# Performance work log

Hardware: AMD Instinct MI355X
Metric: run time of the kernel (lower is better)

The kernel has to match this reference:

```python
import jax, jax.numpy as jnp
import numpy as np

EMBED_DIM = 1024
B, S = 4, 2048

def setup_inputs() -> dict:
    key = jax.random.key(0)
    ks = jax.random.split(key, 9)
    D = EMBED_DIM
    scale = 1.0 / np.sqrt(D)
    scale2 = 1.0 / np.sqrt(2 * D)
    return {
        "classical_state": jax.random.normal(ks[0], (B, S, D), jnp.float32),
        "quantum_state": jax.random.normal(ks[1], (B, S, D), jnp.float32),
        "Wc": jax.random.uniform(ks[2], (D, D), jnp.float32, -scale, scale),
        "bc": jax.random.uniform(ks[3], (D,), jnp.float32, -scale, scale),
        "Wq": jax.random.uniform(ks[4], (D, D), jnp.float32, -scale, scale),
        "bq": jax.random.uniform(ks[5], (D,), jnp.float32, -scale, scale),
        "Wg": jax.random.uniform(ks[6], (D, 2 * D), jnp.float32, -scale2, scale2),
        "bg": jax.random.uniform(ks[7], (D,), jnp.float32, -scale2, scale2),
        "temperature": jnp.array(1.0, jnp.float32),
    }

def reference(classical_state, quantum_state, Wc, bc, Wq, bq, Wg, bg, temperature):
    D = classical_state.shape[-1]
    c_proj = jnp.einsum('bsd,ed->bse', classical_state, Wc) + bc  # [B,S,D]
    q_proj = jnp.einsum('bsd,ed->bse', quantum_state, Wq) + bq    # [B,S,D]
    combined = jnp.concatenate([c_proj, q_proj], axis=-1)         # [B,S,2D]
    interface_state = jax.nn.sigmoid(jnp.einsum('bsf,ef->bse', combined, Wg) + bg)
    similarity = jnp.einsum('bsd,btd->bst', c_proj, q_proj) / jnp.sqrt(jnp.asarray(D, c_proj.dtype))
    attention_weights = jax.nn.softmax(similarity / temperature, axis=-1)  # [B,S,S]
    transfer_state = jnp.einsum('bst,btd->bsd', attention_weights, quantum_state)
    return classical_state + interface_state * transfer_state
```

## Files before the change

kernel.cpp:

```cpp
#include <hip/hip_runtime.h>


typedef unsigned short u16;
typedef unsigned char u8;
typedef __bf16 bf16x8 __attribute__((ext_vector_type(8)));
typedef float f32x4 __attribute__((ext_vector_type(4)));
typedef int i32x4 __attribute__((ext_vector_type(4)));
typedef int i32x8 __attribute__((ext_vector_type(8)));
typedef short short8 __attribute__((ext_vector_type(8)));

__device__ __forceinline__ u16 f2bf(float f) {
    unsigned int x;
    __builtin_memcpy(&x, &f, 4);
    unsigned int r = x + 0x7FFFu + ((x >> 16) & 1u);
    return (u16)(r >> 16);
}
__device__ __forceinline__ float bf2f(u16 u) {
    unsigned int x = ((unsigned int)u) << 16;
    float f;
    __builtin_memcpy(&f, &x, 4);
    return f;
}
__device__ __forceinline__ u8 f2fp8(float f) {
    int p = __builtin_amdgcn_cvt_pk_fp8_f32(f, f, 0, false);
    return (u8)(p & 0xFF);
}

__device__ __forceinline__ void xcd_tile(int& tx, int& ty) {
    const int gx = gridDim.x;
    const int nwg = gx * gridDim.y;
    const int l = blockIdx.x + gx * blockIdx.y;
    const int per = nwg >> 3;
    const int swz = (l & 7) * per + (l >> 3);
    tx = swz % gx;
    ty = swz / gx;
}

#define GLOBAL_TO_LDS16(gp, lp)                                                           \
    __builtin_amdgcn_global_load_lds((const __attribute__((address_space(1))) void*)(gp), \
                                     (__attribute__((address_space(3))) void*)(lp), 16, 0, 0)

__global__ __launch_bounds__(256, 2) void gemm_proj(
    const u16* __restrict__ Ac, const u16* __restrict__ Aq, int lda,
    const u16* __restrict__ Bp, long sBz, int ldb,
    u8* __restrict__ C8, long sCz, int ldc, int K,
    const float* __restrict__ bc, const float* __restrict__ bq) {
    __shared__ __align__(16) u16 As[2][128 * 64];
    __shared__ __align__(16) u16 Bs[2][128 * 64];

    const int tid  = threadIdx.x;
    const int lane = tid & 63;
    const int wave = tid >> 6;
    const int z    = blockIdx.z;

    const u16* a = z ? Aq : Ac;
    const u16* b = Bp + (long)z * sBz;
    const float* bias = z ? bq : bc;

    int tx, ty;
    xcd_tile(tx, ty);
    const int tileM = ty * 128;
    const int tileN = tx * 128;

    const int wm  = wave >> 1;
    const int wn  = wave & 1;
    const int r16 = lane & 15;
    const int kg  = lane >> 4;

    const int srow = lane >> 3;
    const int sgc  = ((lane & 7) ^ (lane >> 3)) * 8;
    const int swb  = r16 & 7;

    auto stage = [&](int buf, int t) {
        const int k0 = t * 64;
#pragma unroll
        for (int p = 0; p < 4; p++) {
            const int rbase = p * 32 + wave * 8;
            GLOBAL_TO_LDS16(a + (long)(tileM + rbase + srow) * lda + k0 + sgc, &As[buf][rbase * 64]);
            GLOBAL_TO_LDS16(b + (long)(tileN + rbase + srow) * ldb + k0 + sgc, &Bs[buf][rbase * 64]);
        }
    };

    f32x4 acc[4][4] = {};

    const int nt = K / 64;
    stage(0, 0);
    stage(1, 1);

    for (int t = 0; t < nt; t++) {
        const int cur = t & 1;
        if (t + 1 < nt) asm volatile("s_waitcnt vmcnt(8)" ::: "memory");
        else            asm volatile("s_waitcnt vmcnt(0)" ::: "memory");
        __builtin_amdgcn_s_barrier();
        asm volatile("" ::: "memory");

        bf16x8 af[2][4], bfr[2][4];
#pragma unroll
        for (int h = 0; h < 2; h++) {
#pragma unroll
            for (int i = 0; i < 4; i++) {
                const int Ra = wm * 64 + i * 16 + r16;
                af[h][i]  = *(const bf16x8*)&As[cur][Ra * 64 + (((h * 4 + kg) ^ swb)) * 8];
                const int Rb = wn * 64 + i * 16 + r16;
                bfr[h][i] = *(const bf16x8*)&Bs[cur][Rb * 64 + (((h * 4 + kg) ^ swb)) * 8];
            }
        }
#pragma unroll
        for (int h = 0; h < 2; h++)
#pragma unroll
            for (int i = 0; i < 4; i++)
#pragma unroll
                for (int j = 0; j < 4; j++)
                    acc[i][j] = __builtin_amdgcn_mfma_f32_16x16x32_bf16(
                        af[h][i], bfr[h][j], acc[i][j], 0, 0, 0);

        asm volatile("" ::: "memory");
        __builtin_amdgcn_s_barrier();
        if (t + 2 < nt) stage(cur, t + 2);
    }

#pragma unroll
    for (int i = 0; i < 4; i++)
#pragma unroll
        for (int j = 0; j < 4; j++) {
            int col = tileN + wn * 64 + j * 16 + r16;
            float bv = bias[col];
#pragma unroll
            for (int v = 0; v < 4; v++) {
                int row = tileM + wm * 64 + i * 16 + kg * 4 + v;
                C8[(long)z * sCz + (long)row * ldc + col] = f2fp8(acc[i][j][v] + bv);
            }
        }
}

template <int MODE>
__device__ __forceinline__ void gemm8_body(
    int tileM, int tileN, int z, int tid,
    const u8* __restrict__ A0, const u8* __restrict__ A1, long sAz, int lda, int kSplit,
    const u8* __restrict__ Bp, long sBz, int ldb,
    void* __restrict__ Cp, long cOff, long sCz, int ldc, int K,
    const float* __restrict__ bias, const float* __restrict__ temp,
    const float* __restrict__ cls, const u16* __restrict__ g16,
    float* __restrict__ lsum, long lSz,
    u8* As, u8* Bs) {
    const int lane = tid & 63;
    const int wave = tid >> 6;

    const u8* a = A0 + (long)z * sAz;
    const u8* b = Bp + (long)z * sBz;

    const int wm  = wave >> 1;
    const int wn  = wave & 1;
    const int r16 = lane & 15;
    const int kg  = lane >> 4;

    const int srow = lane >> 3;
    const int sgc  = ((lane & 7) ^ (lane >> 3)) * 16;

    f32x4 acc[4][4] = {};

    for (int k0 = 0; k0 < K; k0 += 128) {
        const u8* Ap = a;
        int kA = k0;
        if (MODE == 1 && k0 >= kSplit) { Ap = A1; kA = k0 - kSplit; }

#pragma unroll
        for (int p = 0; p < 4; p++) {
            const int rbase = p * 32 + wave * 8;
            GLOBAL_TO_LDS16(Ap + (long)(tileM + rbase + srow) * lda + kA + sgc, &As[rbase * 128]);
            GLOBAL_TO_LDS16(b + (long)(tileN + rbase + srow) * ldb + k0 + sgc, &Bs[rbase * 128]);
        }
        __syncthreads();

        i32x8 af[4];
#pragma unroll
        for (int i = 0; i < 4; i++) {
            const int Ra = wm * 64 + i * 16 + r16;
            const u8* base = &As[Ra * 128];
            *(i32x4*)&af[i]       = *(const i32x4*)&base[(((2 * kg)     ^ (Ra & 7))) * 16];
            *((i32x4*)&af[i] + 1) = *(const i32x4*)&base[(((2 * kg + 1) ^ (Ra & 7))) * 16];
        }
#pragma unroll
        for (int j = 0; j < 4; j++) {
            const int Rb = wn * 64 + j * 16 + r16;
            const u8* base = &Bs[Rb * 128];
            i32x8 bfr;
            *(i32x4*)&bfr       = *(const i32x4*)&base[(((2 * kg)     ^ (Rb & 7))) * 16];
            *((i32x4*)&bfr + 1) = *(const i32x4*)&base[(((2 * kg + 1) ^ (Rb & 7))) * 16];
#pragma unroll
            for (int i = 0; i < 4; i++)
                acc[i][j] = __builtin_amdgcn_mfma_scale_f32_16x16x128_f8f6f4(
                    af[i], bfr, acc[i][j], 0, 0, 0, 127, 0, 127);
        }
        __syncthreads();
    }

    u16*   C16 = (u16*)Cp;
    u8*    C8  = (u8*)Cp;
    float* C32 = (float*)Cp;

    if constexpr (MODE == 2) {
        const float scale = 1.0f / (32.0f * temp[0]);
        u8* Cs = As;
#pragma unroll
        for (int i = 0; i < 4; i++) {
            float rs[4] = {0.f, 0.f, 0.f, 0.f};
#pragma unroll
            for (int j = 0; j < 4; j++) {
                const int lcol = wn * 64 + j * 16 + r16;
#pragma unroll
                for (int v = 0; v < 4; v++) {
                    const int lrow = wm * 64 + i * 16 + kg * 4 + v;
                    float e = __expf(acc[i][j][v] * scale);
                    Cs[lrow * 128 + (lcol ^ ((lrow & 12) << 2))] = f2fp8(e);
                    rs[v] += e;
                }
            }
#pragma unroll
            for (int v = 0; v < 4; v++) {
                float s = rs[v];
#pragma unroll
                for (int off = 1; off < 16; off <<= 1) s += __shfl_xor(s, off, 64);
                if (r16 == 0) {
                    int row = tileM + wm * 64 + i * 16 + kg * 4 + v;
                    atomicAdd(&lsum[(long)z * lSz + row], s);
                }
            }
        }
        __syncthreads();
        const int r  = tid >> 1;
        const int ch = (tid & 1) * 64;
        const int rk = (r >> 2) & 3;
        i32x4 w[4];
#pragma unroll
        for (int m = 0; m < 4; m++)
            w[m] = *(const i32x4*)&Cs[r * 128 + ch + ((m ^ rk) << 4)];
        long base = cOff + (long)z * sCz + (long)(tileM + r) * ldc + tileN + ch;
#pragma unroll
        for (int m = 0; m < 4; m++)
            *(i32x4*)&C8[base + m * 16] = w[m];
    } else {
#pragma unroll
        for (int i = 0; i < 4; i++) {
#pragma unroll
            for (int j = 0; j < 4; j++) {
                int col = tileN + wn * 64 + j * 16 + r16;
                float bv = (MODE == 1) ? bias[col] : 0.0f;
#pragma unroll
                for (int v = 0; v < 4; v++) {
                    int row = tileM + wm * 64 + i * 16 + kg * 4 + v;
                    long idx = cOff + (long)z * sCz + (long)row * ldc + col;
                    float val = acc[i][j][v];
                    if (MODE == 1) {
                        C16[idx] = f2bf(1.0f / (1.0f + __expf(-(val + bv))));
                    } else {
                        float inv = 1.0f / lsum[(long)z * lSz + row];
                        C32[idx] = cls[idx] + bf2f(g16[idx]) * (val * inv);
                    }
                }
            }
        }
    }
}

template <int MODE>
__global__ __launch_bounds__(256, 2) void gemm8(
    const u8* __restrict__ A0, const u8* __restrict__ A1, long sAz, int lda, int kSplit,
    const u8* __restrict__ Bp, long sBz, int ldb,
    void* __restrict__ Cp, long cOff, long sCz, int ldc, int K,
    const float* __restrict__ bias, const float* __restrict__ temp,
    const float* __restrict__ cls, const u16* __restrict__ g16,
    float* __restrict__ lsum, long lSz) {
    __shared__ __align__(16) u8 As[128 * 128];
    __shared__ __align__(16) u8 Bs[128 * 128];
    int tx, ty;
    xcd_tile(tx, ty);
    gemm8_body<MODE>(ty * 128, tx * 128, blockIdx.z, threadIdx.x,
                     A0, A1, sAz, lda, kSplit, Bp, sBz, ldb,
                     Cp, cOff, sCz, ldc, K, bias, temp, cls, g16, lsum, lSz, As, Bs);
}

__global__ __launch_bounds__(256, 2) void gateSim(
    const u8* __restrict__ cp8, const u8* __restrict__ qp8,
    const u8* __restrict__ Wg8, u16* __restrict__ g, const float* __restrict__ bg,
    u8* __restrict__ P8, long sP, const float* __restrict__ temp,
    float* __restrict__ lsum, long lSz,
    long sBD, int D, int S, int nwgSim) {
    __shared__ __align__(16) u8 As[128 * 128];
    __shared__ __align__(16) u8 Bs[128 * 128];
    const int bid = blockIdx.x;
    if (bid < 512) {
        const int swz = (bid & 7) * 64 + (bid >> 3);
        const int tx = swz & 7, ty = swz >> 3;
        gemm8_body<1>(ty * 128, tx * 128, 0, threadIdx.x,
                      cp8, qp8, 0, D, D, Wg8, 0, 2 * D,
                      g, 0, 0, D, 2 * D,
                      bg, nullptr, nullptr, nullptr, nullptr, 0, As, Bs);
    } else {
        const int sb  = bid - 512;
        const int z   = sb / nwgSim;
        const int lid = sb - z * nwgSim;
        const int per = nwgSim >> 3;
        const int swz = (lid & 7) * per + (lid >> 3);
        const int tx = swz & 15, ty = swz >> 4;
        gemm8_body<2>(ty * 128, tx * 128, z, threadIdx.x,
                      cp8, nullptr, sBD, D, 1 << 30, qp8, sBD, D,
                      P8, 0, sP, S, D,
                      nullptr, temp, nullptr, nullptr, lsum, lSz, As, Bs);
    }
}

__global__ __launch_bounds__(256) void prepT(
    const f32x4* __restrict__ cls, const f32x4* __restrict__ qnt,
    const f32x4* __restrict__ Wc, const f32x4* __restrict__ Wq, const f32x4* __restrict__ Wg,
    ushort4* __restrict__ clsB, ushort4* __restrict__ qntB,
    ushort4* __restrict__ WcB, ushort4* __restrict__ WqB, unsigned int* __restrict__ Wg8,
    f32x4* __restrict__ l, long nM, long nW, long nG, long nL,
    const float* __restrict__ Qf, u8* __restrict__ QT, int S, int D) {
    __shared__ __align__(16) u8 tile[64][80];
    const int bid = blockIdx.x;
    if (bid < 2048) {
        long i = (long)bid * 256 + threadIdx.x;
        const long stride = 2048L * 256;
        const long total = 2 * nM + 2 * nW + nG + nL;
        for (; i < total; i += stride) {
            if (i < 2 * nM) {
                long j = (i < nM) ? i : i - nM;
                f32x4 v = (i < nM) ? cls[j] : qnt[j];
                ushort4 o;
                o.x = f2bf(v.x); o.y = f2bf(v.y); o.z = f2bf(v.z); o.w = f2bf(v.w);
                if (i < nM) clsB[j] = o; else qntB[j] = o;
            } else if (i < 2 * nM + 2 * nW) {
                long j = i - 2 * nM;
                long k = (j < nW) ? j : j - nW;
                f32x4 v = (j < nW) ? Wc[k] : Wq[k];
                ushort4 o;
                o.x = f2bf(v.x); o.y = f2bf(v.y); o.z = f2bf(v.z); o.w = f2bf(v.w);
                if (j < nW) WcB[k] = o; else WqB[k] = o;
            } else if (i < 2 * nM + 2 * nW + nG) {
                long j = i - 2 * nM - 2 * nW;
                f32x4 v = Wg[j];
                int w = __builtin_amdgcn_cvt_pk_fp8_f32(v.x, v.y, 0, false);
                w = __builtin_amdgcn_cvt_pk_fp8_f32(v.z, v.w, w, true);
                Wg8[j] = (unsigned int)w;
            } else {
                l[i - 2 * nM - 2 * nW - nG] = (f32x4){0.f, 0.f, 0.f, 0.f};
            }
        }
    } else {
        const int tb = bid - 2048;
        const int bx = tb & 31;
        const int by = (tb >> 5) & 15;
        const int bz = tb >> 9;
        const float* q = Qf + (long)bz * S * D;
        u8* qt = QT + (long)bz * S * D;
        const int t0 = bx * 64, d0 = by * 64;
        {
            const int r  = threadIdx.x >> 2;
            const int dc = (threadIdx.x & 3) * 16;
            const float* src = q + (long)(t0 + r) * D + d0 + dc;
            unsigned int pk[4];
#pragma unroll
            for (int m = 0; m < 4; m++) {
                f32x4 v = *(const f32x4*)(src + 4 * m);
                int w = __builtin_amdgcn_cvt_pk_fp8_f32(v.x, v.y, 0, false);
                w = __builtin_amdgcn_cvt_pk_fp8_f32(v.z, v.w, w, true);
                pk[m] = (unsigned int)w;
            }
            *(i32x4*)&tile[r][dc] = *(i32x4*)pk;
        }
        __syncthreads();
        {
            const int dl = threadIdx.x >> 2;
            const int tc = (threadIdx.x & 3) * 16;
            unsigned int w[4];
#pragma unroll
            for (int m = 0; m < 4; m++) {
                unsigned int x = 0;
#pragma unroll
                for (int k = 0; k < 4; k++)
                    x |= (unsigned int)tile[tc + m * 4 + k][dl] << (8 * k);
                w[m] = x;
            }
            *(i32x4*)&qt[(long)(d0 + dl) * S + t0 + tc] = *(i32x4*)w;
        }
    }
}

extern "C" void kernel_launch(void* const* d_in, const int* in_sizes, int n_in,
                              void* d_out, int out_size, void* d_ws, size_t ws_size,
                              hipStream_t stream) {
    (void)in_sizes; (void)n_in; (void)out_size;

    const float* classical = (const float*)d_in[0];
    const float* quantum   = (const float*)d_in[1];
    const float* Wc        = (const float*)d_in[2];
    const float* bc        = (const float*)d_in[3];
    const float* Wq        = (const float*)d_in[4];
    const float* bq        = (const float*)d_in[5];
    const float* Wg        = (const float*)d_in[6];
    const float* bg        = (const float*)d_in[7];
    const float* temp      = (const float*)d_in[8];
    float* out = (float*)d_out;

    const int B = 4, S = 2048, D = 1024;
    const long MD = (long)B * S * D;

    float* l    = (float*)d_ws;
    u16* Wc_b   = (u16*)(l + (long)B * S);
    u16* Wq_b   = Wc_b + (long)D * D;
    u8*  Wg8    = (u8*)(Wq_b + (long)D * D);
    u16* cls_b  = (u16*)(Wg8 + (long)D * 2 * D);
    u16* qnt_b  = cls_b + MD;
    u8*  cp8    = (u8*)(qnt_b + MD);
    u8*  qp8    = cp8 + MD;
    u8*  qT8    = qp8 + MD;
    u8*  P8     = qT8 + MD;
    u16* g      = cls_b;

    const size_t fixed_bytes = (size_t)B * S * 4 + 2 * (size_t)D * D * 2 +
        (size_t)D * 2 * D + 2 * (size_t)MD * 2 + 3 * (size_t)MD;
    int CH = 128;
    for (int c = 2048; c >= 128; c >>= 1) {
        if (ws_size >= fixed_bytes + (size_t)B * c * S) { CH = c; break; }
    }
    const int chDiv  = CH / 128;
    const int nwgSim = (S / 128) * chDiv;

    dim3 blk(256);

    prepT<<<4096, blk, 0, stream>>>(
        (const f32x4*)classical, (const f32x4*)quantum,
        (const f32x4*)Wc, (const f32x4*)Wq, (const f32x4*)Wg,
        (ushort4*)cls_b, (ushort4*)qnt_b,
        (ushort4*)Wc_b, (ushort4*)Wq_b, (unsigned int*)Wg8,
        (f32x4*)l, MD / 4, (long)D * D / 4, (long)D * 2 * D / 4, (long)B * S / 4,
        quantum, qT8, S, D);

    gemm_proj<<<dim3(D / 128, (B * S) / 128, 2), blk, 0, stream>>>(
        cls_b, qnt_b, D, Wc_b, (long)D * D, D, cp8, MD, D, D, bc, bq);

    gateSim<<<512 + B * nwgSim, blk, 0, stream>>>(
        cp8, qp8, Wg8, g, bg,
        P8, (long)CH * S, temp, l, S,
        (long)S * D, D, S, nwgSim);

    gemm8<4><<<dim3(D / 128, chDiv, B), blk, 0, stream>>>(
        P8, nullptr, (long)CH * S, S, 1 << 30, qT8, (long)D * S, S,
        out, 0, (long)S * D, D, S,
        nullptr, nullptr, classical, g, l, S);

    for (int m0 = CH; m0 < S; m0 += CH) {
        gemm8<2><<<dim3(S / 128, chDiv, B), blk, 0, stream>>>(
            cp8 + (long)m0 * D, nullptr, (long)S * D, D, 1 << 30,
            qp8, (long)S * D, D, P8, 0, (long)CH * S, S, D,
            nullptr, temp, nullptr, nullptr, l + m0, S);
        gemm8<4><<<dim3(D / 128, chDiv, B), blk, 0, stream>>>(
            P8, nullptr, (long)CH * S, S, 1 << 30, qT8, (long)D * S, S,
            out, (long)m0 * D, (long)S * D, D, S,
            nullptr, nullptr, classical, g, l + m0, S);
    }
}
```

Before: 247.7 us.

## Fuse gate, similarity and PV GEMMs into persistent kernel with atomic counters

Adds a persistent 512-block kernel that computes the similarity tiles and gate GEMM, signals completion through global atomic counters, then runs the P·V output GEMM. The output stage spin-waits on the gate counter only before its epilogue, so its main loop can overlap with gate work. This removes the separate launches and the tail bubble between them when the workspace holds the full S×S matrix. It also drops __restrict__ on GEMM arguments and rewrites the fp8 transpose to pack 4-byte columns in shared memory. The cost is a dependency on spin-wait progress: this assumes all 512 blocks are co-resident, otherwise it can deadlock.

```diff
diff --git a/kernel.cpp b/kernel.cpp
--- a/kernel.cpp
+++ b/kernel.cpp
@@ -7,7 +7,6 @@
 typedef float f32x4 __attribute__((ext_vector_type(4)));
 typedef int i32x4 __attribute__((ext_vector_type(4)));
 typedef int i32x8 __attribute__((ext_vector_type(8)));
-typedef short short8 __attribute__((ext_vector_type(8)));
 
 __device__ __forceinline__ u16 f2bf(float f) {
     unsigned int x;
@@ -133,16 +132,16 @@
         }
 }
 
-template <int MODE>
+template <int MODE, bool WAITG>
 __device__ __forceinline__ void gemm8_body(
     int tileM, int tileN, int z, int tid,
-    const u8* __restrict__ A0, const u8* __restrict__ A1, long sAz, int lda, int kSplit,
-    const u8* __restrict__ Bp, long sBz, int ldb,
-    void* __restrict__ Cp, long cOff, long sCz, int ldc, int K,
-    const float* __restrict__ bias, const float* __restrict__ temp,
-    const float* __restrict__ cls, const u16* __restrict__ g16,
-    float* __restrict__ lsum, long lSz,
-    u8* As, u8* Bs) {
+    const u8* A0, const u8* A1, long sAz, int lda, int kSplit,
+    const u8* Bp, long sBz, int ldb,
+    void* Cp, long cOff, long sCz, int ldc, int K,
+    const float* bias, const float* temp,
+    const float* cls, const u16* g16,
+    float* lsum, long lSz,
+    u8* As, u8* Bs, unsigned int* gDone) {
     const int lane = tid & 63;
     const int wave = tid >> 6;
 
@@ -191,6 +190,15 @@
             for (int i = 0; i < 4; i++)
                 acc[i][j] = __builtin_amdgcn_mfma_scale_f32_16x16x128_f8f6f4(
                     af[i], bfr, acc[i][j], 0, 0, 0, 127, 0, 127);
+        }
+        __syncthreads();
+    }
+
+    if constexpr (WAITG) {
+        if (tid == 0) {
+            while (__hip_atomic_load(gDone, __ATOMIC_RELAXED, __HIP_MEMORY_SCOPE_AGENT) < 512u)
+                __builtin_amdgcn_s_sleep(2);
+            __threadfence();
         }
         __syncthreads();
     }
@@ -265,26 +273,27 @@
 
 template <int MODE>
 __global__ __launch_bounds__(256, 2) void gemm8(
-    const u8* __restrict__ A0, const u8* __restrict__ A1, long sAz, int lda, int kSplit,
-    const u8* __restrict__ Bp, long sBz, int ldb,
-    void* __restrict__ Cp, long cOff, long sCz, int ldc, int K,
-    const float* __restrict__ bias, const float* __restrict__ temp,
-    const float* __restrict__ cls, const u16* __restrict__ g16,
-    float* __restrict__ lsum, long lSz) {
+    const u8* A0, const u8* A1, long sAz, int lda, int kSplit,
+    const u8* Bp, long sBz, int ldb,
+    void* Cp, long cOff, long sCz, int ldc, int K,
+    const float* bias, const float* temp,
+    const float* cls, const u16* g16,
+    float* lsum, long lSz) {
     __shared__ __align__(16) u8 As[128 * 128];
     __shared__ __align__(16) u8 Bs[128 * 128];
     int tx, ty;
     xcd_tile(tx, ty);
-    gemm8_body<MODE>(ty * 128, tx * 128, blockIdx.z, threadIdx.x,
-                     A0, A1, sAz, lda, kSplit, Bp, sBz, ldb,
-                     Cp, cOff, sCz, ldc, K, bias, temp, cls, g16, lsum, lSz, As, Bs);
+    gemm8_body<MODE, false>(ty * 128, tx * 128, blockIdx.z, threadIdx.x,
+                            A0, A1, sAz, lda, kSplit, Bp, sBz, ldb,
+                            Cp, cOff, sCz, ldc, K, bias, temp, cls, g16, lsum, lSz,
+                            As, Bs, nullptr);
 }
 
 __global__ __launch_bounds__(256, 2) void gateSim(
-    const u8* __restrict__ cp8, const u8* __restrict__ qp8,
-    const u8* __restrict__ Wg8, u16* __restrict__ g, const float* __restrict__ bg,
-    u8* __restrict__ P8, long sP, const float* __restrict__ temp,
-    float* __restrict__ lsum, long lSz,
+    const u8* cp8, const u8* qp8,
+    const u8* Wg8, u16* g, const float* bg,
+    u8* P8, long sP, const float* temp,
+    float* lsum, long lSz,
     long sBD, int D, int S, int nwgSim) {
     __shared__ __align__(16) u8 As[128 * 128];
     __shared__ __align__(16) u8 Bs[128 * 128];
@@ -292,10 +301,10 @@
     if (bid < 512) {
         const int swz = (bid & 7) * 64 + (bid >> 3);
         const int tx = swz & 7, ty = swz >> 3;
-        gemm8_body<1>(ty * 128, tx * 128, 0, threadIdx.x,
-                      cp8, qp8, 0, D, D, Wg8, 0, 2 * D,
-                      g, 0, 0, D, 2 * D,
-                      bg, nullptr, nullptr, nullptr, nullptr, 0, As, Bs);
+        gemm8_body<1, false>(ty * 128, tx * 128, 0, threadIdx.x,
+                             cp8, qp8, 0, D, D, Wg8, 0, 2 * D,
+                             g, 0, 0, D, 2 * D,
+                             bg, nullptr, nullptr, nullptr, nullptr, 0, As, Bs, nullptr);
     } else {
         const int sb  = bid - 512;
         const int z   = sb / nwgSim;
@@ -303,10 +312,66 @@
         const int per = nwgSim >> 3;
         const int swz = (lid & 7) * per + (lid >> 3);
         const int tx = swz & 15, ty = swz >> 4;
-        gemm8_body<2>(ty * 128, tx * 128, z, threadIdx.x,
-                      cp8, nullptr, sBD, D, 1 << 30, qp8, sBD, D,
-                      P8, 0, sP, S, D,
-                      nullptr, temp, nullptr, nullptr, lsum, lSz, As, Bs);
+        gemm8_body<2, false>(ty * 128, tx * 128, z, threadIdx.x,
+                             cp8, nullptr, sBD, D, 1 << 30, qp8, sBD, D,
+                             P8, 0, sP, S, D,
+                             nullptr, temp, nullptr, nullptr, lsum, lSz, As, Bs, nullptr);
+    }
+}
+
+__global__ __launch_bounds__(256, 2) void megaGSP(
+    const u8* cp8, const u8* qp8, const u8* Wg8, void* g, const float* bg,
+    void* P8, const float* temp, float* lsum,
+    const u8* qT8, const float* cls, void* out,
+    unsigned int* syncc, int D, int S) {
+    __shared__ __align__(16) u8 As[128 * 128];
+    __shared__ __align__(16) u8 Bs[128 * 128];
+    const int b   = blockIdx.x;
+    const int tid = threadIdx.x;
+    const long sBD = (long)S * D;
+
+#pragma unroll 1
+    for (int it = 0; it < 3; it++) {
+        const int k = b + it * 512;
+        if (k < 1024) {
+            const int z = k >> 8, lid = k & 255;
+            const int swz = (lid & 7) * 32 + (lid >> 3);
+            gemm8_body<2, false>((swz >> 4) * 128, (swz & 15) * 128, z, tid,
+                                 cp8, nullptr, sBD, D, 1 << 30, qp8, sBD, D,
+                                 P8, 0, (long)S * S, S, D,
+                                 nullptr, temp, nullptr, nullptr, lsum, S, As, Bs, nullptr);
+            __syncthreads();
+            if (tid == 0)
+                __hip_atomic_fetch_add(&syncc[0], 1u, __ATOMIC_RELEASE, __HIP_MEMORY_SCOPE_AGENT);
+        } else {
+            const int lid = k - 1024;
+            const int swz = (lid & 7) * 64 + (lid >> 3);
+            gemm8_body<1, false>((swz >> 3) * 128, (swz & 7) * 128, 0, tid,
+                                 cp8, qp8, 0, D, D, Wg8, 0, 2 * D,
+                                 g, 0, 0, D, 2 * D,
+                                 bg, nullptr, nullptr, nullptr, nullptr, 0, As, Bs, nullptr);
+            __syncthreads();
+            if (tid == 0)
+                __hip_atomic_fetch_add(&syncc[1], 1u, __ATOMIC_RELEASE, __HIP_MEMORY_SCOPE_AGENT);
+        }
+    }
+
+    if (tid == 0) {
+        while (__hip_atomic_load(&syncc[0], __ATOMIC_RELAXED, __HIP_MEMORY_SCOPE_AGENT) < 1024u)
+            __builtin_amdgcn_s_sleep(2);
+        __threadfence();
+    }
+    __syncthreads();
+
+    {
+        const int z = b >> 7, lid = b & 127;
+        const int swz = (lid & 7) * 16 + (lid >> 3);
+        gemm8_body<4, true>((swz >> 3) * 128, (swz & 7) * 128, z, tid,
+                            (const u8*)P8, nullptr, (long)S * S, S, 1 << 30,
+                            qT8, (long)D * S, S,
+                            out, 0, sBD, D, S,
+                            nullptr, nullptr, cls, (const u16*)g, lsum, S,
+                            As, Bs, &syncc[1]);
     }
 }
 
@@ -316,9 +381,11 @@
     ushort4* __restrict__ clsB, ushort4* __restrict__ qntB,
     ushort4* __restrict__ WcB, ushort4* __restrict__ WqB, unsigned int* __restrict__ Wg8,
     f32x4* __restrict__ l, long nM, long nW, long nG, long nL,
-    const float* __restrict__ Qf, u8* __restrict__ QT, int S, int D) {
-    __shared__ __align__(16) u8 tile[64][80];
+    const float* __restrict__ Qf, u8* __restrict__ QT, int S, int D,
+    unsigned int* __restrict__ syncc) {
+    __shared__ unsigned int tile2[64][17];
     const int bid = blockIdx.x;
+    if (bid == 0 && threadIdx.x < 4) syncc[threadIdx.x] = 0;
     if (bid < 2048) {
         long i = (long)bid * 256 + threadIdx.x;
         const long stride = 2048L * 256;
@@ -356,33 +423,28 @@
         u8* qt = QT + (long)bz * S * D;
         const int t0 = bx * 64, d0 = by * 64;
         {
-            const int r  = threadIdx.x >> 2;
-            const int dc = (threadIdx.x & 3) * 16;
-            const float* src = q + (long)(t0 + r) * D + d0 + dc;
-            unsigned int pk[4];
-#pragma unroll
-            for (int m = 0; m < 4; m++) {
-                f32x4 v = *(const f32x4*)(src + 4 * m);
-                int w = __builtin_amdgcn_cvt_pk_fp8_f32(v.x, v.y, 0, false);
-                w = __builtin_amdgcn_cvt_pk_fp8_f32(v.z, v.w, w, true);
-                pk[m] = (unsigned int)w;
-            }
-            *(i32x4*)&tile[r][dc] = *(i32x4*)pk;
+            const int dg = threadIdx.x & 15;
+            const int tg = threadIdx.x >> 4;
+            unsigned int col[4] = {0u, 0u, 0u, 0u};
+#pragma unroll
+            for (int r = 0; r < 4; r++) {
+                f32x4 v = *(const f32x4*)(q + (long)(t0 + tg * 4 + r) * D + d0 + dg * 4);
+                col[0] |= (unsigned int)f2fp8(v.x) << (8 * r);
+                col[1] |= (unsigned int)f2fp8(v.y) << (8 * r);
+                col[2] |= (unsigned int)f2fp8(v.z) << (8 * r);
+                col[3] |= (unsigned int)f2fp8(v.w) << (8 * r);
+            }
+#pragma unroll
+            for (int j = 0; j < 4; j++) tile2[dg * 4 + j][tg] = col[j];
         }
         __syncthreads();
         {
-            const int dl = threadIdx.x >> 2;
-            const int tc = (threadIdx.x & 3) * 16;
-            unsigned int w[4];
-#pragma unroll
-            for (int m = 0; m < 4; m++) {
-                unsigned int x = 0;
-#pragma unroll
-                for (int k = 0; k < 4; k++)
-                    x |= (unsigned int)tile[tc + m * 4 + k][dl] << (8 * k);
-                w[m] = x;
-            }
-            *(i32x4*)&qt[(long)(d0 + dl) * S + t0 + tc] = *(i32x4*)w;
+            const int dr = threadIdx.x >> 2;
+            const int mq = threadIdx.x & 3;
+            i32x4 w;
+#pragma unroll
+            for (int k = 0; k < 4; k++) w[k] = (int)tile2[dr][mq * 4 + k];
+            *(i32x4*)&qt[(long)(d0 + dr) * S + t0 + mq * 16] = w;
         }
     }
 }
@@ -422,10 +484,9 @@
         (size_t)D * 2 * D + 2 * (size_t)MD * 2 + 3 * (size_t)MD;
     int CH = 128;
     for (int c = 2048; c >= 128; c >>= 1) {
-        if (ws_size >= fixed_bytes + (size_t)B * c * S) { CH = c; break; }
-    }
-    const int chDiv  = CH / 128;
-    const int nwgSim = (S / 128) * chDiv;
+        if (ws_size >= fixed_bytes + (size_t)B * c * S + 64) { CH = c; break; }
+    }
+    unsigned int* syncc = (unsigned int*)(P8 + (size_t)B * CH * S);
 
     dim3 blk(256);
 
@@ -435,29 +496,35 @@
         (ushort4*)cls_b, (ushort4*)qnt_b,
         (ushort4*)Wc_b, (ushort4*)Wq_b, (unsigned int*)Wg8,
         (f32x4*)l, MD / 4, (long)D * D / 4, (long)D * 2 * D / 4, (long)B * S / 4,
-        quantum, qT8, S, D);
+        quantum, qT8, S, D, syncc);
 
     gemm_proj<<<dim3(D / 128, (B * S) / 128, 2), blk, 0, stream>>>(
         cls_b, qnt_b, D, Wc_b, (long)D * D, D, cp8, MD, D, D, bc, bq);
 
-    gateSim<<<512 + B * nwgSim, blk, 0, stream>>>(
-        cp8, qp8, Wg8, g, bg,
-        P8, (long)CH * S, temp, l, S,
-        (long)S * D, D, S, nwgSim);
-
-    gemm8<4><<<dim3(D / 128, chDiv, B), blk, 0, stream>>>(
-        P8, nullptr, (long)CH * S, S, 1 << 30, qT8, (long)D * S, S,
-        out, 0, (long)S * D, D, S,
-        nullptr, nullptr, classical, g, l, S);
-
-    for (int m0 = CH; m0 < S; m0 += CH) {
-        gemm8<2><<<dim3(S / 128, chDiv, B), blk, 0, stream>>>(
-            cp8 + (long)m0 * D, nullptr, (long)S * D, D, 1 << 30,
-            qp8, (long)S * D, D, P8, 0, (long)CH * S, S, D,
-            nullptr, temp, nullptr, nullptr, l + m0, S);
+    if (CH == S) {
+        megaGSP<<<512, blk, 0, stream>>>(
+            cp8, qp8, Wg8, g, bg, P8, temp, l, qT8, classical, out,
+            syncc, D, S);
+    } else {
+        const int chDiv  = CH / 128;
+        const int nwgSim = (S / 128) * chDiv;
+        gateSim<<<512 + B * nwgSim, blk, 0, stream>>>(
+            cp8, qp8, Wg8, g, bg,
+            P8, (long)CH * S, temp, l, S,
+            (long)S * D, D, S, nwgSim);
         gemm8<4><<<dim3(D / 128, chDiv, B), blk, 0, stream>>>(
             P8, nullptr, (long)CH * S, S, 1 << 30, qT8, (long)D * S, S,
-            out, (long)m0 * D, (long)S * D, D, S,
-            nullptr, nullptr, classical, g, l + m0, S);
-    }
-}
+            out, 0, (long)S * D, D, S,
+            nullptr, nullptr, classical, g, l, S);
+        for (int m0 = CH; m0 < S; m0 += CH) {
+            gemm8<2><<<dim3(S / 128, chDiv, B), blk, 0, stream>>>(
+                cp8 + (long)m0 * D, nullptr, (long)S * D, D, 1 << 30,
+                qp8, (long)S * D, D, P8, 0, (long)CH * S, S, D,
+                nullptr, temp, nullptr, nullptr, l + m0, S);
+            gemm8<4><<<dim3(D / 128, chDiv, B), blk, 0, stream>>>(
+                P8, nullptr, (long)CH * S, S, 1 << 30, qT8, (long)D * S, S,
+                out, (long)m0 * D, (long)S * D, D, S,
+                nullptr, nullptr, classical, g, l + m0, S);
+        }
+    }
+}
```

New measurement: 365.6 us. 47.6% more time.

## Move quantum-state FP8 transpose from prep kernel into gate/similarity launch

Applied to the files above, without the earlier changes.

The transpose-and-quantize of the quantum state to FP8 (qT8) moves out of the prep kernel and runs as extra trailing blocks of the gateSim launch, with a new LDS layout that packs four tokens per word and reads 16-byte rows. The prep kernel shrinks to the elementwise conversions, so the transpose work can overlap with the gate and similarity GEMM tail instead of lengthening the first kernel. The __restrict__ qualifiers are also dropped from the GEMM signatures, which may change how the compiler schedules loads. The extra blocks could contend with the GEMM tiles for CUs, and the transpose still has to finish before the later PV GEMM, which reads qT8.

```diff
diff --git a/kernel.cpp b/kernel.cpp
--- a/kernel.cpp
+++ b/kernel.cpp
@@ -7,7 +7,6 @@
 typedef float f32x4 __attribute__((ext_vector_type(4)));
 typedef int i32x4 __attribute__((ext_vector_type(4)));
 typedef int i32x8 __attribute__((ext_vector_type(8)));
-typedef short short8 __attribute__((ext_vector_type(8)));
 
 __device__ __forceinline__ u16 f2bf(float f) {
     unsigned int x;
@@ -136,12 +135,12 @@
 template <int MODE>
 __device__ __forceinline__ void gemm8_body(
     int tileM, int tileN, int z, int tid,
-    const u8* __restrict__ A0, const u8* __restrict__ A1, long sAz, int lda, int kSplit,
-    const u8* __restrict__ Bp, long sBz, int ldb,
-    void* __restrict__ Cp, long cOff, long sCz, int ldc, int K,
-    const float* __restrict__ bias, const float* __restrict__ temp,
-    const float* __restrict__ cls, const u16* __restrict__ g16,
-    float* __restrict__ lsum, long lSz,
+    const u8* A0, const u8* A1, long sAz, int lda, int kSplit,
+    const u8* Bp, long sBz, int ldb,
+    void* Cp, long cOff, long sCz, int ldc, int K,
+    const float* bias, const float* temp,
+    const float* cls, const u16* g16,
+    float* lsum, long lSz,
     u8* As, u8* Bs) {
     const int lane = tid & 63;
     const int wave = tid >> 6;
@@ -265,12 +264,12 @@
 
 template <int MODE>
 __global__ __launch_bounds__(256, 2) void gemm8(
-    const u8* __restrict__ A0, const u8* __restrict__ A1, long sAz, int lda, int kSplit,
-    const u8* __restrict__ Bp, long sBz, int ldb,
-    void* __restrict__ Cp, long cOff, long sCz, int ldc, int K,
-    const float* __restrict__ bias, const float* __restrict__ temp,
-    const float* __restrict__ cls, const u16* __restrict__ g16,
-    float* __restrict__ lsum, long lSz) {
+    const u8* A0, const u8* A1, long sAz, int lda, int kSplit,
+    const u8* Bp, long sBz, int ldb,
+    void* Cp, long cOff, long sCz, int ldc, int K,
+    const float* bias, const float* temp,
+    const float* cls, const u16* g16,
+    float* lsum, long lSz) {
     __shared__ __align__(16) u8 As[128 * 128];
     __shared__ __align__(16) u8 Bs[128 * 128];
     int tx, ty;
@@ -281,32 +280,68 @@
 }
 
 __global__ __launch_bounds__(256, 2) void gateSim(
-    const u8* __restrict__ cp8, const u8* __restrict__ qp8,
-    const u8* __restrict__ Wg8, u16* __restrict__ g, const float* __restrict__ bg,
-    u8* __restrict__ P8, long sP, const float* __restrict__ temp,
-    float* __restrict__ lsum, long lSz,
-    long sBD, int D, int S, int nwgSim) {
+    const u8* cp8, const u8* qp8,
+    const u8* Wg8, u16* g, const float* bg,
+    u8* P8, long sP, const float* temp,
+    float* lsum, long lSz,
+    long sBD, int D, int S, int nwgSim,
+    const float* Qf, u8* qT8) {
     __shared__ __align__(16) u8 As[128 * 128];
     __shared__ __align__(16) u8 Bs[128 * 128];
     const int bid = blockIdx.x;
+    const int tid = threadIdx.x;
+    const int gemmEnd = 512 + 4 * nwgSim;
     if (bid < 512) {
         const int swz = (bid & 7) * 64 + (bid >> 3);
         const int tx = swz & 7, ty = swz >> 3;
-        gemm8_body<1>(ty * 128, tx * 128, 0, threadIdx.x,
+        gemm8_body<1>(ty * 128, tx * 128, 0, tid,
                       cp8, qp8, 0, D, D, Wg8, 0, 2 * D,
                       g, 0, 0, D, 2 * D,
                       bg, nullptr, nullptr, nullptr, nullptr, 0, As, Bs);
-    } else {
+    } else if (bid < gemmEnd) {
         const int sb  = bid - 512;
         const int z   = sb / nwgSim;
         const int lid = sb - z * nwgSim;
         const int per = nwgSim >> 3;
         const int swz = (lid & 7) * per + (lid >> 3);
         const int tx = swz & 15, ty = swz >> 4;
-        gemm8_body<2>(ty * 128, tx * 128, z, threadIdx.x,
+        gemm8_body<2>(ty * 128, tx * 128, z, tid,
                       cp8, nullptr, sBD, D, 1 << 30, qp8, sBD, D,
                       P8, 0, sP, S, D,
                       nullptr, temp, nullptr, nullptr, lsum, lSz, As, Bs);
+    } else {
+        const int tb = bid - gemmEnd;
+        const int bx = tb & 31;
+        const int by = (tb >> 5) & 15;
+        const int bz = tb >> 9;
+        unsigned int (*tile2)[17] = (unsigned int(*)[17])As;
+        const float* q = Qf + (long)bz * S * D;
+        u8* qt = qT8 + (long)bz * S * D;
+        const int t0 = bx * 64, d0 = by * 64;
+        {
+            const int dg = tid & 15;
+            const int tg = tid >> 4;
+            unsigned int col[4] = {0u, 0u, 0u, 0u};
+#pragma unroll
+            for (int r = 0; r < 4; r++) {
+                f32x4 v = *(const f32x4*)(q + (long)(t0 + tg * 4 + r) * D + d0 + dg * 4);
+                col[0] |= (unsigned int)f2fp8(v.x) << (8 * r);
+                col[1] |= (unsigned int)f2fp8(v.y) << (8 * r);
+                col[2] |= (unsigned int)f2fp8(v.z) << (8 * r);
+                col[3] |= (unsigned int)f2fp8(v.w) << (8 * r);
+            }
+#pragma unroll
+            for (int j = 0; j < 4; j++) tile2[dg * 4 + j][tg] = col[j];
+        }
+        __syncthreads();
+        {
+            const int dr = tid >> 2;
+            const int mq = tid & 3;
+            i32x4 w;
+#pragma unroll
+            for (int k = 0; k < 4; k++) w[k] = (int)tile2[dr][mq * 4 + k];
+            *(i32x4*)&qt[(long)(d0 + dr) * S + t0 + mq * 16] = w;
+        }
     }
 }
 
@@ -315,74 +350,32 @@
     const f32x4* __restrict__ Wc, const f32x4* __restrict__ Wq, const f32x4* __restrict__ Wg,
     ushort4* __restrict__ clsB, ushort4* __restrict__ qntB,
     ushort4* __restrict__ WcB, ushort4* __restrict__ WqB, unsigned int* __restrict__ Wg8,
-    f32x4* __restrict__ l, long nM, long nW, long nG, long nL,
-    const float* __restrict__ Qf, u8* __restrict__ QT, int S, int D) {
-    __shared__ __align__(16) u8 tile[64][80];
-    const int bid = blockIdx.x;
-    if (bid < 2048) {
-        long i = (long)bid * 256 + threadIdx.x;
-        const long stride = 2048L * 256;
-        const long total = 2 * nM + 2 * nW + nG + nL;
-        for (; i < total; i += stride) {
-            if (i < 2 * nM) {
-                long j = (i < nM) ? i : i - nM;
-                f32x4 v = (i < nM) ? cls[j] : qnt[j];
-                ushort4 o;
-                o.x = f2bf(v.x); o.y = f2bf(v.y); o.z = f2bf(v.z); o.w = f2bf(v.w);
-                if (i < nM) clsB[j] = o; else qntB[j] = o;
-            } else if (i < 2 * nM + 2 * nW) {
-                long j = i - 2 * nM;
-                long k = (j < nW) ? j : j - nW;
-                f32x4 v = (j < nW) ? Wc[k] : Wq[k];
-                ushort4 o;
-                o.x = f2bf(v.x); o.y = f2bf(v.y); o.z = f2bf(v.z); o.w = f2bf(v.w);
-                if (j < nW) WcB[k] = o; else WqB[k] = o;
-            } else if (i < 2 * nM + 2 * nW + nG) {
-                long j = i - 2 * nM - 2 * nW;
-                f32x4 v = Wg[j];
-                int w = __builtin_amdgcn_cvt_pk_fp8_f32(v.x, v.y, 0, false);
-                w = __builtin_amdgcn_cvt_pk_fp8_f32(v.z, v.w, w, true);
-                Wg8[j] = (unsigned int)w;
-            } else {
-                l[i - 2 * nM - 2 * nW - nG] = (f32x4){0.f, 0.f, 0.f, 0.f};
-            }
-        }
-    } else {
-        const int tb = bid - 2048;
-        const int bx = tb & 31;
-        const int by = (tb >> 5) & 15;
-        const int bz = tb >> 9;
-        const float* q = Qf + (long)bz * S * D;
-        u8* qt = QT + (long)bz * S * D;
-        const int t0 = bx * 64, d0 = by * 64;
-        {
-            const int r  = threadIdx.x >> 2;
-            const int dc = (threadIdx.x & 3) * 16;
-            const float* src = q + (long)(t0 + r) * D + d0 + dc;
-            unsigned int pk[4];
-#pragma unroll
-            for (int m = 0; m < 4; m++) {
-                f32x4 v = *(const f32x4*)(src + 4 * m);
-                int w = __builtin_amdgcn_cvt_pk_fp8_f32(v.x, v.y, 0, false);
-                w = __builtin_amdgcn_cvt_pk_fp8_f32(v.z, v.w, w, true);
-                pk[m] = (unsigned int)w;
-            }
-            *(i32x4*)&tile[r][dc] = *(i32x4*)pk;
-        }
-        __syncthreads();
-        {
-            const int dl = threadIdx.x >> 2;
-            const int tc = (threadIdx.x & 3) * 16;
-            unsigned int w[4];
-#pragma unroll
-            for (int m = 0; m < 4; m++) {
-                unsigned int x = 0;
-#pragma unroll
-                for (int k = 0; k < 4; k++)
-                    x |= (unsigned int)tile[tc + m * 4 + k][dl] << (8 * k);
-                w[m] = x;
-            }
-            *(i32x4*)&qt[(long)(d0 + dl) * S + t0 + tc] = *(i32x4*)w;
+    f32x4* __restrict__ l, long nM, long nW, long nG, long nL) {
+    long i = (long)blockIdx.x * 256 + threadIdx.x;
+    const long stride = (long)gridDim.x * 256;
+    const long total = 2 * nM + 2 * nW + nG + nL;
+    for (; i < total; i += stride) {
+        if (i < 2 * nM) {
+            long j = (i < nM) ? i : i - nM;
+            f32x4 v = (i < nM) ? cls[j] : qnt[j];
+            ushort4 o;
+            o.x = f2bf(v.x); o.y = f2bf(v.y); o.z = f2bf(v.z); o.w = f2bf(v.w);
+            if (i < nM) clsB[j] = o; else qntB[j] = o;
+        } else if (i < 2 * nM + 2 * nW) {
+            long j = i - 2 * nM;
+            long k = (j < nW) ? j : j - nW;
+            f32x4 v = (j < nW) ? Wc[k] : Wq[k];
+            ushort4 o;
+            o.x = f2bf(v.x); o.y = f2bf(v.y); o.z = f2bf(v.z); o.w = f2bf(v.w);
+            if (j < nW) WcB[k] = o; else WqB[k] = o;
+        } else if (i < 2 * nM + 2 * nW + nG) {
+            long j = i - 2 * nM - 2 * nW;
+            f32x4 v = Wg[j];
+            int w = __builtin_amdgcn_cvt_pk_fp8_f32(v.x, v.y, 0, false);
+            w = __builtin_amdgcn_cvt_pk_fp8_f32(v.z, v.w, w, true);
+            Wg8[j] = (unsigned int)w;
+        } else {
+            l[i - 2 * nM - 2 * nW - nG] = (f32x4){0.f, 0.f, 0.f, 0.f};
         }
     }
 }
@@ -429,21 +422,21 @@
 
     dim3 blk(256);
 
-    prepT<<<4096, blk, 0, stream>>>(
+    prepT<<<2048, blk, 0, stream>>>(
         (const f32x4*)classical, (const f32x4*)quantum,
         (const f32x4*)Wc, (const f32x4*)Wq, (const f32x4*)Wg,
         (ushort4*)cls_b, (ushort4*)qnt_b,
         (ushort4*)Wc_b, (ushort4*)Wq_b, (unsigned int*)Wg8,
-        (f32x4*)l, MD / 4, (long)D * D / 4, (long)D * 2 * D / 4, (long)B * S / 4,
-        quantum, qT8, S, D);
+        (f32x4*)l, MD / 4, (long)D * D / 4, (long)D * 2 * D / 4, (long)B * S / 4);
 
     gemm_proj<<<dim3(D / 128, (B * S) / 128, 2), blk, 0, stream>>>(
         cls_b, qnt_b, D, Wc_b, (long)D * D, D, cp8, MD, D, D, bc, bq);
 
-    gateSim<<<512 + B * nwgSim, blk, 0, stream>>>(
+    gateSim<<<512 + B * nwgSim + 2048, blk, 0, stream>>>(
         cp8, qp8, Wg8, g, bg,
         P8, (long)CH * S, temp, l, S,
-        (long)S * D, D, S, nwgSim);
+        (long)S * D, D, S, nwgSim,
+        quantum, qT8);
 
     gemm8<4><<<dim3(D / 128, chDiv, B), blk, 0, stream>>>(
         P8, nullptr, (long)CH * S, S, 1 << 30, qT8, (long)D * S, S,
```

After: 263.3 us. 1.06x slower.
